# Kernel optimization log

Measured on AMD Instinct MI355X. Metric: run time of the kernel, lower is better.

Reference implementation:

```python
import jax, jax.numpy as jnp
import numpy as np

NUM_HEADS = 8  # init kwarg num_heads


def setup_inputs() -> dict:
    key = jax.random.key(0)
    ks = jax.random.split(key, 6)
    B, H, W, C, ws = 16, 128, 128, 256, 8
    hd = C // NUM_HEADS
    s = 0.02
    return {
        "x": jax.random.normal(ks[0], (B, H * W, C), jnp.float32),
        "qkv_w": jax.random.normal(ks[1], (3 * C, C), jnp.float32) * s,
        "qkv_b": jnp.zeros((3 * C,), jnp.float32),
        "proj_w": jax.random.normal(ks[2], (C, C), jnp.float32) * s,
        "proj_b": jnp.zeros((C,), jnp.float32),
        "rel_pos_h": jax.random.normal(ks[3], (2 * ws - 1, hd), jnp.float32) * s,
        "rel_pos_w": jax.random.normal(ks[4], (2 * ws - 1, hd), jnp.float32) * s,
        "H": 128,
        "W": 128,
    }


def reference(x, qkv_w, qkv_b, proj_w, proj_b, rel_pos_h, rel_pos_w, H, W):
    # WindowAttention forward (H, W divisible by window -> pad is a no-op).
    ws = (rel_pos_h.shape[0] + 1) // 2          # window size (8)
    B, N, C = x.shape
    heads = NUM_HEADS
    hd = C // heads
    scale = hd ** -0.5

    # window_partition: (B, H, W, C) -> (B*nWh*nWw, ws*ws, C)
    xw = x.reshape(B, H // ws, ws, W // ws, ws, C)
    xw = xw.transpose(0, 1, 3, 2, 4, 5).reshape(-1, ws * ws, C)
    Bw, Nw, _ = xw.shape

    qkv = xw @ qkv_w.T + qkv_b                   # (Bw, Nw, 3C)
    qkv = qkv.reshape(Bw, Nw, 3, heads, hd).transpose(2, 0, 3, 1, 4)
    q, k, v = qkv[0], qkv[1], qkv[2]             # (Bw, heads, Nw, hd)

    attn = jnp.einsum('bhqd,bhkd->bhqk', q * scale, k)

    # gather-based spatial relative position bias (calc_rel_pos_spatial, q==k shape)
    idx = jnp.arange(ws)[:, None] - jnp.arange(ws)[None, :] + (ws - 1)  # (ws, ws)
    Rh = rel_pos_h[idx]                          # (ws, ws, hd)
    Rw = rel_pos_w[idx]                          # (ws, ws, hd)
    r_q = q.reshape(Bw, heads, ws, ws, hd)
    rel_h = jnp.einsum('byhwc,hkc->byhwk', r_q, Rh)   # (Bw, heads, ws, ws, ws)
    rel_w_ = jnp.einsum('byhwc,wkc->byhwk', r_q, Rw)  # (Bw, heads, ws, ws, ws)
    attn = (attn.reshape(Bw, heads, ws, ws, ws, ws)
            + rel_h[:, :, :, :, :, None]
            + rel_w_[:, :, :, :, None, :]).reshape(Bw, heads, Nw, Nw)

    attn = jax.nn.softmax(attn, axis=-1)
    attn = jnp.where(jnp.isinf(attn) | jnp.isnan(attn), 0.0, attn)

    out = jnp.einsum('bhqk,bhkd->bhqd', attn, v)
    out = out.transpose(0, 2, 1, 3).reshape(Bw, Nw, C)
    out = out @ proj_w.T + proj_b

    # window_reverse: (Bw, Nw, C) -> (B, H, W, C) -> (B, N, C)
    out = out.reshape(B, H // ws, W // ws, ws, ws, C)
    out = out.transpose(0, 1, 3, 2, 4, 5).reshape(B, H, W, C)
    return out.reshape(B, N, C)
```

## Files before the change

### kernel.cpp

```cpp
#include <hip/hip_runtime.h>
#include <hip/hip_bf16.h>
#include <cstdint>
#include <cstddef>

typedef __bf16 bft;
typedef __bf16 bf16x8 __attribute__((ext_vector_type(8)));
typedef __bf16 bf16x4 __attribute__((ext_vector_type(4)));
typedef float  f32x4  __attribute__((ext_vector_type(4)));

#define MFMA(a, b, c) __builtin_amdgcn_mfma_f32_16x16x32_bf16(a, b, c, 0, 0, 0)

constexpr float SCALE = 0.17677669529663689f;
constexpr float INVS  = 5.656854249492381f;

__global__ __launch_bounds__(256) void cvt_kernel(const float* __restrict__ s,
                                                  bft* __restrict__ d, int n) {
  int stride = gridDim.x * blockDim.x;
  for (int i = blockIdx.x * blockDim.x + threadIdx.x; i * 4 < n; i += stride) {
    const float4 v = *reinterpret_cast<const float4*>(s + (size_t)i * 4);
    bf16x4 o = {(bft)v.x, (bft)v.y, (bft)v.z, (bft)v.w};
    *reinterpret_cast<bf16x4*>(d + (size_t)i * 4) = o;
  }
}

__global__ __launch_bounds__(256, 2) void win_fused(
    const float* __restrict__ X, const bft* __restrict__ Wq,
    const float* __restrict__ Bq, const bft* __restrict__ Wp,
    const float* __restrict__ Bp, const float* __restrict__ rph,
    const float* __restrict__ rpw, float* __restrict__ Out) {
  __shared__ alignas(16) bft QK[18432];
  __shared__ alignas(16) bft VO[20480];

  const int t = threadIdx.x, lane = t & 63, wv = t >> 6;
  const int l15 = lane & 15, l4 = lane >> 4;
  const int win = blockIdx.x;
  const int b = win >> 8, wh = (win >> 4) & 15, ww = win & 15;
  const float* xw =
      X + ((size_t)b * 16384 + (size_t)(wh * 8) * 128 + ww * 8) * 256;

  bf16x8 rhf = {}, rwf = {};
  if (l15 < 15) {
    const float* th = rph + l15 * 32 + l4 * 8;
    const float* tw = rpw + l15 * 32 + l4 * 8;
#pragma unroll
    for (int j = 0; j < 8; ++j) {
      rhf[j] = (bft)(th[j] * INVS);
      rwf[j] = (bft)(tw[j] * INVS);
    }
  }

  const int qb = wv * 4608, kb = qb + 2304;

#pragma unroll 1
  for (int p = 0; p < 2; ++p) {
    const int h = wv + p * 4;
    const int vb = h * 2560;

    bf16x8 af[4][8];
#pragma unroll
    for (int m = 0; m < 4; ++m) {
      const int tok = m * 16 + l15;
      const float* rowp = xw + (size_t)((tok >> 3) * 128 + (tok & 7)) * 256;
#pragma unroll
      for (int kk = 0; kk < 8; ++kk) {
        const float* cp = rowp + kk * 32 + l4 * 8;
        float4 a = *reinterpret_cast<const float4*>(cp);
        float4 c2 = *reinterpret_cast<const float4*>(cp + 4);
        bf16x8 f = {(bft)a.x, (bft)a.y, (bft)a.z, (bft)a.w,
                    (bft)c2.x, (bft)c2.y, (bft)c2.z, (bft)c2.w};
        af[m][kk] = f;
      }
    }

#pragma unroll
    for (int comp = 0; comp < 3; ++comp) {
#pragma unroll
      for (int half = 0; half < 2; ++half) {
        const int n0 = comp * 256 + h * 32 + half * 16;
        bf16x8 bw[8];
#pragma unroll
        for (int kk = 0; kk < 8; ++kk)
          bw[kk] = *reinterpret_cast<const bf16x8*>(
              &Wq[(size_t)(n0 + l15) * 256 + kk * 32 + l4 * 8]);
        f32x4 acc[4] = {};
#pragma unroll
        for (int kk = 0; kk < 8; ++kk)
#pragma unroll
          for (int m = 0; m < 4; ++m) acc[m] = MFMA(af[m][kk], bw[kk], acc[m]);
        const float bias = Bq[n0 + l15];
        if (comp == 0) {
#pragma unroll
          for (int m = 0; m < 4; ++m)
#pragma unroll
            for (int r = 0; r < 4; ++r)
              QK[qb + (m * 16 + l4 * 4 + r) * 36 + half * 16 + l15] =
                  (bft)((acc[m][r] + bias) * SCALE);
        } else if (comp == 1) {
#pragma unroll
          for (int m = 0; m < 4; ++m)
#pragma unroll
            for (int r = 0; r < 4; ++r)
              QK[kb + (m * 16 + l4 * 4 + r) * 36 + half * 16 + l15] =
                  (bft)(acc[m][r] + bias);
        } else {
#pragma unroll
          for (int m = 0; m < 4; ++m) {
            bf16x4 pk = {(bft)(acc[m][0] + bias), (bft)(acc[m][1] + bias),
                         (bft)(acc[m][2] + bias), (bft)(acc[m][3] + bias)};
            *reinterpret_cast<bf16x4*>(
                &VO[vb + (half * 16 + l15) * 68 + m * 16 + l4 * 4]) = pk;
          }
        }
      }
    }

    bf16x8 qf[4], kf[4];
#pragma unroll
    for (int i = 0; i < 4; ++i) {
      bf16x4 lo, hi;
      lo = *reinterpret_cast<const bf16x4*>(&QK[qb + (i * 16 + l15) * 36 + l4 * 8]);
      hi = *reinterpret_cast<const bf16x4*>(&QK[qb + (i * 16 + l15) * 36 + l4 * 8 + 4]);
      qf[i] = __builtin_shufflevector(lo, hi, 0, 1, 2, 3, 4, 5, 6, 7);
      lo = *reinterpret_cast<const bf16x4*>(&QK[kb + (i * 16 + l15) * 36 + l4 * 8]);
      hi = *reinterpret_cast<const bf16x4*>(&QK[kb + (i * 16 + l15) * 36 + l4 * 8 + 4]);
      kf[i] = __builtin_shufflevector(lo, hi, 0, 1, 2, 3, 4, 5, 6, 7);
    }
    f32x4 s[4][4], gh[4], gw[4];
#pragma unroll
    for (int i = 0; i < 4; ++i) {
      f32x4 z = {};
      gh[i] = MFMA(qf[i], rhf, z);
      gw[i] = MFMA(qf[i], rwf, z);
#pragma unroll
      for (int j = 0; j < 4; ++j) {
        f32x4 z2 = {};
        s[i][j] = MFMA(qf[i], kf[j], z2);
      }
    }
#pragma unroll
    for (int i = 0; i < 4; ++i)
#pragma unroll
      for (int r = 0; r < 4; ++r) {
        const int row = i * 16 + l4 * 4 + r;
        const int qy = row >> 3, qx = row & 7;
        const float bwv = __shfl(gw[i][r], (lane & 48) + (qx + 7 - (l15 & 7)));
        float v0[4], mx = -3.0e38f;
#pragma unroll
        for (int j = 0; j < 4; ++j) {
          const float bh =
              __shfl(gh[i][r], (lane & 48) + (qy + 7 - (j * 2 + (l15 >> 3))));
          v0[j] = s[i][j][r] + bh + bwv;
          mx = fmaxf(mx, v0[j]);
        }
        mx = fmaxf(mx, __shfl_xor(mx, 1));
        mx = fmaxf(mx, __shfl_xor(mx, 2));
        mx = fmaxf(mx, __shfl_xor(mx, 4));
        mx = fmaxf(mx, __shfl_xor(mx, 8));
        float sum = 0.f;
#pragma unroll
        for (int j = 0; j < 4; ++j) {
          v0[j] = __expf(v0[j] - mx);
          sum += v0[j];
        }
        sum += __shfl_xor(sum, 1);
        sum += __shfl_xor(sum, 2);
        sum += __shfl_xor(sum, 4);
        sum += __shfl_xor(sum, 8);
        const float inv = 1.0f / sum;
#pragma unroll
        for (int j = 0; j < 4; ++j)
          QK[qb + row * 68 + j * 16 + l15] = (bft)(v0[j] * inv);
      }
    bf16x8 pf[4][2], vf[2][2];
#pragma unroll
    for (int i = 0; i < 4; ++i)
#pragma unroll
      for (int kc = 0; kc < 2; ++kc) {
        bf16x4 lo = *reinterpret_cast<const bf16x4*>(
            &QK[qb + (i * 16 + l15) * 68 + kc * 32 + l4 * 8]);
        bf16x4 hi = *reinterpret_cast<const bf16x4*>(
            &QK[qb + (i * 16 + l15) * 68 + kc * 32 + l4 * 8 + 4]);
        pf[i][kc] = __builtin_shufflevector(lo, hi, 0, 1, 2, 3, 4, 5, 6, 7);
      }
#pragma unroll
    for (int j2 = 0; j2 < 2; ++j2)
#pragma unroll
      for (int kc = 0; kc < 2; ++kc) {
        bf16x4 lo = *reinterpret_cast<const bf16x4*>(
            &VO[vb + (j2 * 16 + l15) * 68 + kc * 32 + l4 * 8]);
        bf16x4 hi = *reinterpret_cast<const bf16x4*>(
            &VO[vb + (j2 * 16 + l15) * 68 + kc * 32 + l4 * 8 + 4]);
        vf[j2][kc] = __builtin_shufflevector(lo, hi, 0, 1, 2, 3, 4, 5, 6, 7);
      }
    f32x4 o[4][2] = {};
#pragma unroll
    for (int i = 0; i < 4; ++i)
#pragma unroll
      for (int j2 = 0; j2 < 2; ++j2) {
        o[i][j2] = MFMA(pf[i][0], vf[j2][0], o[i][j2]);
        o[i][j2] = MFMA(pf[i][1], vf[j2][1], o[i][j2]);
      }
#pragma unroll
    for (int i = 0; i < 4; ++i)
#pragma unroll
      for (int j2 = 0; j2 < 2; ++j2)
#pragma unroll
        for (int r = 0; r < 4; ++r)
          VO[vb + (i * 16 + l4 * 4 + r) * 40 + j2 * 16 + l15] =
              (bft)o[i][j2][r];
  }
  __syncthreads();

  f32x4 po[4][4] = {};
#pragma unroll
  for (int sH = 0; sH < 8; ++sH) {
    bf16x8 oa[4];
#pragma unroll
    for (int m = 0; m < 4; ++m)
      oa[m] = *reinterpret_cast<const bf16x8*>(
          &VO[sH * 2560 + (m * 16 + l15) * 40 + l4 * 8]);
#pragma unroll
    for (int n = 0; n < 4; ++n) {
      bf16x8 wb = *reinterpret_cast<const bf16x8*>(
          &Wp[(size_t)(wv * 64 + n * 16 + l15) * 256 + sH * 32 + l4 * 8]);
#pragma unroll
      for (int m = 0; m < 4; ++m) po[m][n] = MFMA(oa[m], wb, po[m][n]);
    }
  }
  float pbias[4];
#pragma unroll
  for (int n = 0; n < 4; ++n) pbias[n] = Bp[wv * 64 + n * 16 + l15];
  float* ob = Out + ((size_t)b * 16384 + (size_t)(wh * 8) * 128 + ww * 8) * 256;
#pragma unroll
  for (int m = 0; m < 4; ++m)
#pragma unroll
    for (int r = 0; r < 4; ++r) {
      const int tok = m * 16 + l4 * 4 + r;
      float* og = ob + ((size_t)(tok >> 3) * 128 + (tok & 7)) * 256;
#pragma unroll
      for (int n = 0; n < 4; ++n)
        og[wv * 64 + n * 16 + l15] = po[m][n][r] + pbias[n];
    }
}

extern "C" void kernel_launch(void* const* d_in, const int* in_sizes, int n_in,
                              void* d_out, int out_size, void* d_ws,
                              size_t ws_size, hipStream_t stream) {
  const float* x      = (const float*)d_in[0];
  const float* qkv_w  = (const float*)d_in[1];
  const float* qkv_b  = (const float*)d_in[2];
  const float* proj_w = (const float*)d_in[3];
  const float* proj_b = (const float*)d_in[4];
  const float* rph    = (const float*)d_in[5];
  const float* rpw    = (const float*)d_in[6];
  float* out = (float*)d_out;

  if (ws_size < 524288) return;
  bft* qw = (bft*)d_ws;
  bft* pw = (bft*)((char*)d_ws + 393216);

  cvt_kernel<<<192, 256, 0, stream>>>(qkv_w, qw, 196608);
  cvt_kernel<<<64, 256, 0, stream>>>(proj_w, pw, 65536);
  win_fused<<<4096, 256, 0, stream>>>(x, qw, qkv_b, pw, proj_b, rph, rpw, out);
}
```

Baseline: 875.1 us.

## Split output projection into separate GEMM kernel and stream QKV K-loop

The fused window-attention kernel is split in two when the workspace is large enough. The attention kernel writes per-head bf16 outputs to a global workspace and drops the in-kernel projection, which cuts LDS use and allows 3 blocks per CU. A separate tiled MFMA GEMM then applies the projection, adds the bias and performs the window-reverse scatter. The QKV projection now streams X per k-step into per-tile accumulators instead of holding all A fragments, which lowers register pressure but re-reads X twice per head pass. This adds about 128MB of global write and read traffic for the intermediate and one extra launch.

```diff
diff --git a/kernel.cpp b/kernel.cpp
--- a/kernel.cpp
+++ b/kernel.cpp
@@ -9,6 +9,7 @@
 typedef float  f32x4  __attribute__((ext_vector_type(4)));
 
 #define MFMA(a, b, c) __builtin_amdgcn_mfma_f32_16x16x32_bf16(a, b, c, 0, 0, 0)
+#define LDS_FENCE() asm volatile("s_waitcnt lgkmcnt(0)" ::: "memory")
 
 constexpr float SCALE = 0.17677669529663689f;
 constexpr float INVS  = 5.656854249492381f;
@@ -23,13 +24,14 @@
   }
 }
 
-__global__ __launch_bounds__(256, 2) void win_fused(
+template <int SPLIT>
+__global__ __launch_bounds__(256, SPLIT ? 3 : 2) void win_k(
     const float* __restrict__ X, const bft* __restrict__ Wq,
     const float* __restrict__ Bq, const bft* __restrict__ Wp,
     const float* __restrict__ Bp, const float* __restrict__ rph,
-    const float* __restrict__ rpw, float* __restrict__ Out) {
-  __shared__ alignas(16) bft QK[18432];
-  __shared__ alignas(16) bft VO[20480];
+    const float* __restrict__ rpw, float* __restrict__ Out,
+    bft* __restrict__ Ows) {
+  __shared__ alignas(16) bft lds[SPLIT ? 27136 : 38912];
 
   const int t = threadIdx.x, lane = t & 63, wv = t >> 6;
   const int l15 = lane & 15, l4 = lane >> 4;
@@ -51,78 +53,93 @@
 
   const int qb = wv * 4608, kb = qb + 2304;
 
+  auto load_af = [&](int kk, bf16x8 af[4]) {
+#pragma unroll
+    for (int m = 0; m < 4; ++m) {
+      const int tok = m * 16 + l15;
+      const float* cp =
+          xw + (size_t)((tok >> 3) * 128 + (tok & 7)) * 256 + kk * 32 + l4 * 8;
+      float4 a = *reinterpret_cast<const float4*>(cp);
+      float4 c2 = *reinterpret_cast<const float4*>(cp + 4);
+      bf16x8 f = {(bft)a.x, (bft)a.y, (bft)a.z, (bft)a.w,
+                  (bft)c2.x, (bft)c2.y, (bft)c2.z, (bft)c2.w};
+      af[m] = f;
+    }
+  };
+
 #pragma unroll 1
   for (int p = 0; p < 2; ++p) {
     const int h = wv + p * 4;
-    const int vb = h * 2560;
-
-    bf16x8 af[4][8];
-#pragma unroll
-    for (int m = 0; m < 4; ++m) {
-      const int tok = m * 16 + l15;
-      const float* rowp = xw + (size_t)((tok >> 3) * 128 + (tok & 7)) * 256;
-#pragma unroll
+    const int vb = SPLIT ? (18432 + wv * 2176) : (18432 + h * 2560);
+
+    {
+      f32x4 acc[4][4] = {};
+#pragma unroll 2
       for (int kk = 0; kk < 8; ++kk) {
-        const float* cp = rowp + kk * 32 + l4 * 8;
-        float4 a = *reinterpret_cast<const float4*>(cp);
-        float4 c2 = *reinterpret_cast<const float4*>(cp + 4);
-        bf16x8 f = {(bft)a.x, (bft)a.y, (bft)a.z, (bft)a.w,
-                    (bft)c2.x, (bft)c2.y, (bft)c2.z, (bft)c2.w};
-        af[m][kk] = f;
-      }
-    }
-
-#pragma unroll
-    for (int comp = 0; comp < 3; ++comp) {
-#pragma unroll
-      for (int half = 0; half < 2; ++half) {
-        const int n0 = comp * 256 + h * 32 + half * 16;
-        bf16x8 bw[8];
-#pragma unroll
-        for (int kk = 0; kk < 8; ++kk)
-          bw[kk] = *reinterpret_cast<const bf16x8*>(
+        bf16x8 af[4];
+        load_af(kk, af);
+#pragma unroll
+        for (int tq = 0; tq < 4; ++tq) {
+          const int n0 = (tq >> 1) * 256 + h * 32 + (tq & 1) * 16;
+          bf16x8 bw = *reinterpret_cast<const bf16x8*>(
               &Wq[(size_t)(n0 + l15) * 256 + kk * 32 + l4 * 8]);
-        f32x4 acc[4] = {};
-#pragma unroll
-        for (int kk = 0; kk < 8; ++kk)
-#pragma unroll
-          for (int m = 0; m < 4; ++m) acc[m] = MFMA(af[m][kk], bw[kk], acc[m]);
-        const float bias = Bq[n0 + l15];
-        if (comp == 0) {
-#pragma unroll
-          for (int m = 0; m < 4; ++m)
-#pragma unroll
-            for (int r = 0; r < 4; ++r)
-              QK[qb + (m * 16 + l4 * 4 + r) * 36 + half * 16 + l15] =
-                  (bft)((acc[m][r] + bias) * SCALE);
-        } else if (comp == 1) {
-#pragma unroll
-          for (int m = 0; m < 4; ++m)
-#pragma unroll
-            for (int r = 0; r < 4; ++r)
-              QK[kb + (m * 16 + l4 * 4 + r) * 36 + half * 16 + l15] =
-                  (bft)(acc[m][r] + bias);
-        } else {
-#pragma unroll
-          for (int m = 0; m < 4; ++m) {
-            bf16x4 pk = {(bft)(acc[m][0] + bias), (bft)(acc[m][1] + bias),
-                         (bft)(acc[m][2] + bias), (bft)(acc[m][3] + bias)};
-            *reinterpret_cast<bf16x4*>(
-                &VO[vb + (half * 16 + l15) * 68 + m * 16 + l4 * 4]) = pk;
-          }
-        }
-      }
-    }
+#pragma unroll
+          for (int m = 0; m < 4; ++m) acc[tq][m] = MFMA(af[m], bw, acc[tq][m]);
+        }
+      }
+#pragma unroll
+      for (int tq = 0; tq < 4; ++tq) {
+        const int comp = tq >> 1, half = tq & 1;
+        const float bias = Bq[comp * 256 + h * 32 + half * 16 + l15];
+        const int base = (comp == 0) ? qb : kb;
+        const float sc = (comp == 0) ? SCALE : 1.0f;
+#pragma unroll
+        for (int m = 0; m < 4; ++m)
+#pragma unroll
+          for (int r = 0; r < 4; ++r)
+            lds[base + (m * 16 + l4 * 4 + r) * 36 + half * 16 + l15] =
+                (bft)((acc[tq][m][r] + bias) * sc);
+      }
+    }
+
+    {
+      f32x4 av[2][4] = {};
+#pragma unroll 2
+      for (int kk = 0; kk < 8; ++kk) {
+        bf16x8 af[4];
+        load_af(kk, af);
+#pragma unroll
+        for (int tv = 0; tv < 2; ++tv) {
+          const int n0 = 512 + h * 32 + tv * 16;
+          bf16x8 bw = *reinterpret_cast<const bf16x8*>(
+              &Wq[(size_t)(n0 + l15) * 256 + kk * 32 + l4 * 8]);
+#pragma unroll
+          for (int m = 0; m < 4; ++m) av[tv][m] = MFMA(af[m], bw, av[tv][m]);
+        }
+      }
+#pragma unroll
+      for (int tv = 0; tv < 2; ++tv) {
+        const float bias = Bq[512 + h * 32 + tv * 16 + l15];
+#pragma unroll
+        for (int m = 0; m < 4; ++m) {
+          bf16x4 pk = {(bft)(av[tv][m][0] + bias), (bft)(av[tv][m][1] + bias),
+                       (bft)(av[tv][m][2] + bias), (bft)(av[tv][m][3] + bias)};
+          *reinterpret_cast<bf16x4*>(
+              &lds[vb + (tv * 16 + l15) * 68 + m * 16 + l4 * 4]) = pk;
+        }
+      }
+    }
+    LDS_FENCE();
 
     bf16x8 qf[4], kf[4];
 #pragma unroll
     for (int i = 0; i < 4; ++i) {
       bf16x4 lo, hi;
-      lo = *reinterpret_cast<const bf16x4*>(&QK[qb + (i * 16 + l15) * 36 + l4 * 8]);
-      hi = *reinterpret_cast<const bf16x4*>(&QK[qb + (i * 16 + l15) * 36 + l4 * 8 + 4]);
+      lo = *reinterpret_cast<const bf16x4*>(&lds[qb + (i * 16 + l15) * 36 + l4 * 8]);
+      hi = *reinterpret_cast<const bf16x4*>(&lds[qb + (i * 16 + l15) * 36 + l4 * 8 + 4]);
       qf[i] = __builtin_shufflevector(lo, hi, 0, 1, 2, 3, 4, 5, 6, 7);
-      lo = *reinterpret_cast<const bf16x4*>(&QK[kb + (i * 16 + l15) * 36 + l4 * 8]);
-      hi = *reinterpret_cast<const bf16x4*>(&QK[kb + (i * 16 + l15) * 36 + l4 * 8 + 4]);
+      lo = *reinterpret_cast<const bf16x4*>(&lds[kb + (i * 16 + l15) * 36 + l4 * 8]);
+      hi = *reinterpret_cast<const bf16x4*>(&lds[kb + (i * 16 + l15) * 36 + l4 * 8 + 4]);
       kf[i] = __builtin_shufflevector(lo, hi, 0, 1, 2, 3, 4, 5, 6, 7);
     }
     f32x4 s[4][4], gh[4], gw[4];
@@ -169,17 +186,18 @@
         const float inv = 1.0f / sum;
 #pragma unroll
         for (int j = 0; j < 4; ++j)
-          QK[qb + row * 68 + j * 16 + l15] = (bft)(v0[j] * inv);
-      }
+          lds[qb + row * 68 + j * 16 + l15] = (bft)(v0[j] * inv);
+      }
+    LDS_FENCE();
     bf16x8 pf[4][2], vf[2][2];
 #pragma unroll
     for (int i = 0; i < 4; ++i)
 #pragma unroll
       for (int kc = 0; kc < 2; ++kc) {
         bf16x4 lo = *reinterpret_cast<const bf16x4*>(
-            &QK[qb + (i * 16 + l15) * 68 + kc * 32 + l4 * 8]);
+            &lds[qb + (i * 16 + l15) * 68 + kc * 32 + l4 * 8]);
         bf16x4 hi = *reinterpret_cast<const bf16x4*>(
-            &QK[qb + (i * 16 + l15) * 68 + kc * 32 + l4 * 8 + 4]);
+            &lds[qb + (i * 16 + l15) * 68 + kc * 32 + l4 * 8 + 4]);
         pf[i][kc] = __builtin_shufflevector(lo, hi, 0, 1, 2, 3, 4, 5, 6, 7);
       }
 #pragma unroll
@@ -187,9 +205,9 @@
 #pragma unroll
       for (int kc = 0; kc < 2; ++kc) {
         bf16x4 lo = *reinterpret_cast<const bf16x4*>(
-            &VO[vb + (j2 * 16 + l15) * 68 + kc * 32 + l4 * 8]);
+            &lds[vb + (j2 * 16 + l15) * 68 + kc * 32 + l4 * 8]);
         bf16x4 hi = *reinterpret_cast<const bf16x4*>(
-            &VO[vb + (j2 * 16 + l15) * 68 + kc * 32 + l4 * 8 + 4]);
+            &lds[vb + (j2 * 16 + l15) * 68 + kc * 32 + l4 * 8 + 4]);
         vf[j2][kc] = __builtin_shufflevector(lo, hi, 0, 1, 2, 3, 4, 5, 6, 7);
       }
     f32x4 o[4][2] = {};
@@ -200,47 +218,122 @@
         o[i][j2] = MFMA(pf[i][0], vf[j2][0], o[i][j2]);
         o[i][j2] = MFMA(pf[i][1], vf[j2][1], o[i][j2]);
       }
-#pragma unroll
-    for (int i = 0; i < 4; ++i)
-#pragma unroll
-      for (int j2 = 0; j2 < 2; ++j2)
-#pragma unroll
-        for (int r = 0; r < 4; ++r)
-          VO[vb + (i * 16 + l4 * 4 + r) * 40 + j2 * 16 + l15] =
-              (bft)o[i][j2][r];
-  }
-  __syncthreads();
-
-  f32x4 po[4][4] = {};
-#pragma unroll
-  for (int sH = 0; sH < 8; ++sH) {
-    bf16x8 oa[4];
+    if (SPLIT) {
+      bft* ob = Ows + (size_t)win * 16384 + h * 32;
+#pragma unroll
+      for (int i = 0; i < 4; ++i)
+#pragma unroll
+        for (int j2 = 0; j2 < 2; ++j2)
+#pragma unroll
+          for (int r = 0; r < 4; ++r)
+            ob[(size_t)(i * 16 + l4 * 4 + r) * 256 + j2 * 16 + l15] =
+                (bft)o[i][j2][r];
+    } else {
+#pragma unroll
+      for (int i = 0; i < 4; ++i)
+#pragma unroll
+        for (int j2 = 0; j2 < 2; ++j2)
+#pragma unroll
+          for (int r = 0; r < 4; ++r)
+            lds[vb + (i * 16 + l4 * 4 + r) * 40 + j2 * 16 + l15] =
+                (bft)o[i][j2][r];
+    }
+  }
+
+  if (!SPLIT) {
+    __syncthreads();
+    f32x4 po[4][4] = {};
+#pragma unroll
+    for (int sH = 0; sH < 8; ++sH) {
+      bf16x8 oa[4];
+#pragma unroll
+      for (int m = 0; m < 4; ++m)
+        oa[m] = *reinterpret_cast<const bf16x8*>(
+            &lds[18432 + sH * 2560 + (m * 16 + l15) * 40 + l4 * 8]);
+#pragma unroll
+      for (int n = 0; n < 4; ++n) {
+        bf16x8 wb = *reinterpret_cast<const bf16x8*>(
+            &Wp[(size_t)(wv * 64 + n * 16 + l15) * 256 + sH * 32 + l4 * 8]);
+#pragma unroll
+        for (int m = 0; m < 4; ++m) po[m][n] = MFMA(oa[m], wb, po[m][n]);
+      }
+    }
+    float pbias[4];
+#pragma unroll
+    for (int n = 0; n < 4; ++n) pbias[n] = Bp[wv * 64 + n * 16 + l15];
+    float* ob =
+        Out + ((size_t)b * 16384 + (size_t)(wh * 8) * 128 + ww * 8) * 256;
 #pragma unroll
     for (int m = 0; m < 4; ++m)
-      oa[m] = *reinterpret_cast<const bf16x8*>(
-          &VO[sH * 2560 + (m * 16 + l15) * 40 + l4 * 8]);
-#pragma unroll
-    for (int n = 0; n < 4; ++n) {
-      bf16x8 wb = *reinterpret_cast<const bf16x8*>(
-          &Wp[(size_t)(wv * 64 + n * 16 + l15) * 256 + sH * 32 + l4 * 8]);
-#pragma unroll
-      for (int m = 0; m < 4; ++m) po[m][n] = MFMA(oa[m], wb, po[m][n]);
-    }
-  }
-  float pbias[4];
-#pragma unroll
-  for (int n = 0; n < 4; ++n) pbias[n] = Bp[wv * 64 + n * 16 + l15];
-  float* ob = Out + ((size_t)b * 16384 + (size_t)(wh * 8) * 128 + ww * 8) * 256;
-#pragma unroll
-  for (int m = 0; m < 4; ++m)
+#pragma unroll
+      for (int r = 0; r < 4; ++r) {
+        const int tok = m * 16 + l4 * 4 + r;
+        float* og = ob + ((size_t)(tok >> 3) * 128 + (tok & 7)) * 256;
+#pragma unroll
+        for (int n = 0; n < 4; ++n)
+          og[wv * 64 + n * 16 + l15] = po[m][n][r] + pbias[n];
+      }
+  }
+}
+
+__global__ __launch_bounds__(256) void proj_gemm(const bft* __restrict__ A,
+    const bft* __restrict__ Bm, const float* __restrict__ bias,
+    float* __restrict__ Out) {
+  constexpr int RS = 72;
+  __shared__ alignas(16) bft As[128 * RS];
+  __shared__ alignas(16) bft Bs[128 * RS];
+  const int t = threadIdx.x;
+  const int lane = t & 63, wv = t >> 6;
+  const int wy = wv >> 1, wx = wv & 1;
+  const int l15 = lane & 15, l4 = lane >> 4;
+  const int m0 = blockIdx.x * 128, n0 = blockIdx.y * 128;
+  const int srow = t >> 3, sc = (t & 7) * 8;
+  f32x4 acc[4][4] = {};
+  for (int k0 = 0; k0 < 256; k0 += 64) {
+#pragma unroll
+    for (int i2 = 0; i2 < 4; ++i2) {
+      int r = i2 * 32 + srow;
+      *reinterpret_cast<bf16x8*>(&As[r * RS + sc]) =
+          *reinterpret_cast<const bf16x8*>(&A[(size_t)(m0 + r) * 256 + k0 + sc]);
+      *reinterpret_cast<bf16x8*>(&Bs[r * RS + sc]) =
+          *reinterpret_cast<const bf16x8*>(&Bm[(size_t)(n0 + r) * 256 + k0 + sc]);
+    }
+    __syncthreads();
+#pragma unroll
+    for (int kc = 0; kc < 2; ++kc) {
+      bf16x8 af[4], bfr[4];
+#pragma unroll
+      for (int i = 0; i < 4; ++i)
+        af[i] = *reinterpret_cast<const bf16x8*>(
+            &As[(wy * 64 + i * 16 + l15) * RS + kc * 32 + l4 * 8]);
+#pragma unroll
+      for (int j = 0; j < 4; ++j)
+        bfr[j] = *reinterpret_cast<const bf16x8*>(
+            &Bs[(wx * 64 + j * 16 + l15) * RS + kc * 32 + l4 * 8]);
+#pragma unroll
+      for (int i = 0; i < 4; ++i)
+#pragma unroll
+        for (int j = 0; j < 4; ++j) acc[i][j] = MFMA(af[i], bfr[j], acc[i][j]);
+    }
+    __syncthreads();
+  }
+  const int colb = n0 + wx * 64;
+#pragma unroll
+  for (int i = 0; i < 4; ++i) {
 #pragma unroll
     for (int r = 0; r < 4; ++r) {
-      const int tok = m * 16 + l4 * 4 + r;
-      float* og = ob + ((size_t)(tok >> 3) * 128 + (tok & 7)) * 256;
-#pragma unroll
-      for (int n = 0; n < 4; ++n)
-        og[wv * 64 + n * 16 + l15] = po[m][n][r] + pbias[n];
-    }
+      int row = m0 + wy * 64 + i * 16 + l4 * 4 + r;
+      int win = row >> 6, tok = row & 63;
+      int b = win >> 8, wh = (win >> 4) & 15, ww = win & 15;
+      int y = tok >> 3, x = tok & 7;
+      size_t g = ((size_t)b << 14) + ((size_t)(wh * 8 + y) << 7) + (ww * 8 + x);
+#pragma unroll
+      for (int j = 0; j < 4; ++j) {
+        int col = colb + j * 16 + l15;
+        Out[g * 256 + col] = acc[i][j][r] + bias[col];
+      }
+    }
+  }
 }
 
 extern "C" void kernel_launch(void* const* d_in, const int* in_sizes, int n_in,
@@ -255,11 +348,21 @@
   const float* rpw    = (const float*)d_in[6];
   float* out = (float*)d_out;
 
+  constexpr size_t O_OFF = 524288;
+  constexpr size_t NEED_SPLIT = O_OFF + 134217728ull;
   if (ws_size < 524288) return;
   bft* qw = (bft*)d_ws;
   bft* pw = (bft*)((char*)d_ws + 393216);
+  bft* Ows = (bft*)((char*)d_ws + O_OFF);
 
   cvt_kernel<<<192, 256, 0, stream>>>(qkv_w, qw, 196608);
   cvt_kernel<<<64, 256, 0, stream>>>(proj_w, pw, 65536);
-  win_fused<<<4096, 256, 0, stream>>>(x, qw, qkv_b, pw, proj_b, rph, rpw, out);
+  if (ws_size >= NEED_SPLIT) {
+    win_k<1><<<4096, 256, 0, stream>>>(x, qw, qkv_b, pw, proj_b, rph, rpw,
+                                       out, Ows);
+    proj_gemm<<<dim3(2048, 2), 256, 0, stream>>>(Ows, pw, proj_b, out);
+  } else {
+    win_k<0><<<4096, 256, 0, stream>>>(x, qw, qkv_b, pw, proj_b, rph, rpw,
+                                       out, Ows);
+  }
 }
```

Result: slower. 1.386 ms (+58.4%).
